# Kernel optimization log

Measured on AMD Instinct MI355X. Metric: run time of the kernel, lower is better.

## Reference

```python
import jax, jax.numpy as jnp
import numpy as np

D_MODEL = 1024
N_HEADS = 16
HEAD_DIM = D_MODEL // N_HEADS
NEG_INF = -1e10


def setup_inputs() -> dict:
    key = jax.random.key(0)
    ks = jax.random.split(key, 6)
    B, S = 2, 2048
    x = jax.random.normal(ks[0], (B, S, D_MODEL), dtype=jnp.float32)
    mask = jnp.ones((B, S), dtype=jnp.int32)
    scale_w = 1.0 / np.sqrt(D_MODEL)
    Wq = jax.random.normal(ks[1], (D_MODEL, D_MODEL), dtype=jnp.float32) * scale_w
    Wk = jax.random.normal(ks[2], (D_MODEL, D_MODEL), dtype=jnp.float32) * scale_w
    Wv = jax.random.normal(ks[3], (D_MODEL, D_MODEL), dtype=jnp.float32) * scale_w
    Wo = jax.random.normal(ks[4], (D_MODEL, D_MODEL), dtype=jnp.float32) * scale_w
    bq = jnp.zeros((D_MODEL,), jnp.float32)
    bk = jnp.zeros((D_MODEL,), jnp.float32)
    bv = jnp.zeros((D_MODEL,), jnp.float32)
    bo = jnp.zeros((D_MODEL,), jnp.float32)
    return {"x": x, "mask": mask, "Wq": Wq, "bq": bq, "Wk": Wk, "bk": bk,
            "Wv": Wv, "bv": bv, "Wo": Wo, "bo": bo}


def reference(x, mask, Wq, bq, Wk, bk, Wv, bv, Wo, bo):
    B, S, _ = x.shape
    # Linear projections (torch Linear: y = x @ W.T + b)
    Q = x @ Wq.T + bq
    K = x @ Wk.T + bk
    V = x @ Wv.T + bv
    # [B, H, S, Dh]
    Q = Q.reshape(B, S, N_HEADS, HEAD_DIM).transpose(0, 2, 1, 3)
    K = K.reshape(B, S, N_HEADS, HEAD_DIM).transpose(0, 2, 1, 3)
    V = V.reshape(B, S, N_HEADS, HEAD_DIM).transpose(0, 2, 1, 3)
    scale = jnp.sqrt(jnp.float32(HEAD_DIM))
    energy = jnp.einsum('bhqd,bhkd->bhqk', Q, K) / scale  # [B,H,S,S]
    # mask: [B,S] -> broadcast over heads and query dim (keys masked)
    m = mask[:, None, None, :]  # [B,1,1,S]
    energy = jnp.where(m == 0, jnp.float32(NEG_INF), energy)
    attention = jax.nn.softmax(energy, axis=-1)
    # dropout in eval mode = identity
    out = jnp.einsum('bhqk,bhkd->bhqd', attention, V)  # [B,H,S,Dh]
    out = out.transpose(0, 2, 1, 3).reshape(B, S, D_MODEL)
    return out @ Wo.T + bo
```

## Files before the change

### kernel.cpp

```cpp
#include <hip/hip_runtime.h>
#include <hip/hip_bf16.h>

typedef __hip_bfloat16 bf16;
typedef __attribute__((ext_vector_type(8))) short s8v;
typedef __attribute__((ext_vector_type(4))) float f4v;

#define D_MODEL 1024
#define S_LEN   2048
#define BATCH   2
#define NH      16
#define HD      64
#define M_TOTAL 4096
#define NT      (S_LEN / 64)

__device__ __forceinline__ void gll16(const bf16* g, bf16* l) {
    __builtin_amdgcn_global_load_lds(
        (const __attribute__((address_space(1))) void*)g,
        (__attribute__((address_space(3))) void*)l, 16, 0, 0);
}

__global__ __launch_bounds__(256) void cvt_bf16x8(const float* __restrict__ s,
                                                  bf16* __restrict__ d, int n) {
    int i = (blockIdx.x * 256 + threadIdx.x) * 8;
    if (i < n) {
        float4 a = *(const float4*)(s + i);
        float4 b = *(const float4*)(s + i + 4);
        union { bf16 h[8]; uint4 u; } p;
        p.h[0] = __float2bfloat16(a.x); p.h[1] = __float2bfloat16(a.y);
        p.h[2] = __float2bfloat16(a.z); p.h[3] = __float2bfloat16(a.w);
        p.h[4] = __float2bfloat16(b.x); p.h[5] = __float2bfloat16(b.y);
        p.h[6] = __float2bfloat16(b.z); p.h[7] = __float2bfloat16(b.w);
        *(uint4*)(d + i) = p.u;
    }
}

struct WPtrs { const float* s0; const float* s1; const float* s2; const float* s3;
               bf16* d0; bf16* d1; bf16* d2; bf16* d3; };

__global__ __launch_bounds__(256) void cvt_w(WPtrs p) {
    const float* s; bf16* d;
    switch (blockIdx.y) {
        case 0:  s = p.s0; d = p.d0; break;
        case 1:  s = p.s1; d = p.d1; break;
        case 2:  s = p.s2; d = p.d2; break;
        default: s = p.s3; d = p.d3; break;
    }
    int i = (blockIdx.x * 256 + threadIdx.x) * 8;
    float4 a = *(const float4*)(s + i);
    float4 b = *(const float4*)(s + i + 4);
    union { bf16 h[8]; uint4 u; } q;
    q.h[0] = __float2bfloat16(a.x); q.h[1] = __float2bfloat16(a.y);
    q.h[2] = __float2bfloat16(a.z); q.h[3] = __float2bfloat16(a.w);
    q.h[4] = __float2bfloat16(b.x); q.h[5] = __float2bfloat16(b.y);
    q.h[6] = __float2bfloat16(b.z); q.h[7] = __float2bfloat16(b.w);
    *(uint4*)(d + i) = q.u;
}

template<int TM, int TN>
__device__ __forceinline__ void gemm_main(const bf16* __restrict__ A,
                                          const bf16* __restrict__ W,
                                          bf16* As, bf16* Bs,
                                          int bm, int bn,
                                          f4v (&acc)[TM/32][TN/32])
{
    constexpr int FM = TM / 32, FN = TN / 32;
    constexpr int CALLS_A = TM / 16, CALLS = (TM + TN) / 16, PW = CALLS / 4;
    const int t = threadIdx.x, wv = t >> 6, lane = t & 63;
    const int quad = lane >> 4, l15 = lane & 15;
    const int wm = (wv >> 1) * (TM / 2), wn = (wv & 1) * (TN / 2);
    const int lr = lane >> 2, lc = (lane & 3) * 8;

    auto STAGE = [&](int buf, int k0) {
        #pragma unroll
        for (int c = 0; c < PW; ++c) {
            const int cc = wv * PW + c;
            if (cc < CALLS_A) {
                gll16(A + (size_t)(bm + cc * 16 + lr) * D_MODEL + k0 + lc,
                      As + buf * (TM * 32) + cc * 16 * 32);
            } else {
                const int r2 = cc - CALLS_A;
                gll16(W + (size_t)(bn + r2 * 16 + lr) * D_MODEL + k0 + lc,
                      Bs + buf * (TN * 32) + r2 * 16 * 32);
            }
        }
    };

    STAGE(0, 0);
    __syncthreads();
    int cur = 0;

    for (int k0 = 0; k0 < D_MODEL; k0 += 32) {
        if (k0 + 32 < D_MODEL) STAGE(cur ^ 1, k0 + 32);

        const bf16* ab = As + cur * (TM * 32);
        const bf16* bb = Bs + cur * (TN * 32);
        s8v af[FM], bfv[FN];
        #pragma unroll
        for (int i = 0; i < FM; ++i)
            af[i] = *(const s8v*)(ab + (wm + i * 16 + l15) * 32 + quad * 8);
        #pragma unroll
        for (int j = 0; j < FN; ++j)
            bfv[j] = *(const s8v*)(bb + (wn + j * 16 + l15) * 32 + quad * 8);
        __builtin_amdgcn_s_setprio(1);
        #pragma unroll
        for (int i = 0; i < FM; ++i)
            #pragma unroll
            for (int j = 0; j < FN; ++j)
                acc[i][j] = __builtin_amdgcn_mfma_f32_16x16x32_bf16(af[i], bfv[j], acc[i][j], 0, 0, 0);
        __builtin_amdgcn_s_setprio(0);

        __syncthreads();
        cur ^= 1;
    }
}

__global__ __launch_bounds__(256) void gemm_qkv(
    const bf16* __restrict__ x,
    const bf16* __restrict__ Wq, const bf16* __restrict__ Wk, const bf16* __restrict__ Wv,
    const float* __restrict__ bq, const float* __restrict__ bk, const float* __restrict__ bv,
    bf16* __restrict__ Qb, bf16* __restrict__ Kb, bf16* __restrict__ Vtb)
{
    __shared__ __align__(16) char smem[4 * 64 * 72 * 2];
    bf16* As = (bf16*)smem;
    bf16* Bs = (bf16*)(smem + 2 * 128 * 32 * 2);
    bf16 (*Tw)[64][72] = (bf16(*)[64][72])smem;

    const int z = blockIdx.z;
    const bf16*  W    = (z == 0) ? Wq : (z == 1) ? Wk : Wv;
    const float* bias = (z == 0) ? bq : (z == 1) ? bk : bv;
    bf16*        out  = (z == 0) ? Qb : (z == 1) ? Kb : Vtb;
    const int bm = blockIdx.y * 128, bn = blockIdx.x * 128;

    f4v acc[4][4] = {};
    gemm_main<128, 128>(x, W, As, Bs, bm, bn, acc);

    const int t = threadIdx.x, wv = t >> 6, lane = t & 63;
    const int quad = lane >> 4, l15 = lane & 15;
    const int wm = (wv >> 1) * 64, wn = (wv & 1) * 64;

    if (z == 2) {
        __syncthreads();
        #pragma unroll
        for (int j = 0; j < 4; ++j) {
            const int col = bn + wn + j * 16 + l15;
            const float bv_ = bias[col];
            #pragma unroll
            for (int i = 0; i < 4; ++i) {
                #pragma unroll
                for (int rp = 0; rp < 4; rp += 2) {
                    union { bf16 h[2]; unsigned u; } p2;
                    p2.h[0] = __float2bfloat16(acc[i][j][rp]     + bv_);
                    p2.h[1] = __float2bfloat16(acc[i][j][rp + 1] + bv_);
                    *(unsigned*)&Tw[wv][j * 16 + l15][i * 16 + quad * 4 + rp] = p2.u;
                }
            }
        }
        const int bb = (bm + wm) >> 11, s0 = (bm + wm) & 2047;
        #pragma unroll
        for (int p = 0; p < 8; ++p) {
            const int dl = p * 8 + (lane >> 3);
            const int sl = (lane & 7) * 8;
            const int col = bn + wn + dl;
            const int h = col >> 6, d = col & 63;
            uint4 v = *(const uint4*)&Tw[wv][dl][sl];
            *(uint4*)&out[(((size_t)(bb * NH + h)) * HD + d) * S_LEN + s0 + sl] = v;
        }
    } else {
        #pragma unroll
        for (int j = 0; j < 4; ++j) {
            const int col = bn + wn + j * 16 + l15;
            const float bv_ = bias[col];
            const int h = col >> 6, d = col & 63;
            #pragma unroll
            for (int i = 0; i < 4; ++i) {
                #pragma unroll
                for (int r = 0; r < 4; ++r) {
                    const int row = bm + wm + i * 16 + quad * 4 + r;
                    const int b = row >> 11, s = row & 2047;
                    const float v = acc[i][j][r] + bv_;
                    out[(((size_t)(b * NH + h)) * S_LEN + s) * HD + d] = __float2bfloat16(v);
                }
            }
        }
    }
}

__global__ __launch_bounds__(256) void gemm_out(
    const bf16* __restrict__ Ob, const bf16* __restrict__ Wo,
    const float* __restrict__ bo, float* __restrict__ out)
{
    __shared__ __align__(16) bf16 As[2][64 * 32];
    __shared__ __align__(16) bf16 Bs[2][128 * 32];
    const int bm = blockIdx.y * 64, bn = blockIdx.x * 128;

    f4v acc[2][4] = {};
    gemm_main<64, 128>(Ob, Wo, &As[0][0], &Bs[0][0], bm, bn, acc);

    const int t = threadIdx.x, wv = t >> 6, lane = t & 63;
    const int quad = lane >> 4, l15 = lane & 15;
    const int wm = (wv >> 1) * 32, wn = (wv & 1) * 64;
    #pragma unroll
    for (int j = 0; j < 4; ++j) {
        const int col = bn + wn + j * 16 + l15;
        const float bv_ = bo[col];
        #pragma unroll
        for (int i = 0; i < 2; ++i)
            #pragma unroll
            for (int r = 0; r < 4; ++r) {
                const int row = bm + wm + i * 16 + quad * 4 + r;
                out[(size_t)row * D_MODEL + col] = acc[i][j][r] + bv_;
            }
    }
}

__global__ __launch_bounds__(256) void attn_mfma(
    const bf16* __restrict__ Q, const bf16* __restrict__ K,
    const bf16* __restrict__ Vt, const int* __restrict__ mask,
    bf16* __restrict__ O)
{
    __shared__ __align__(16) bf16 Ks[2][64][64];
    __shared__ __align__(16) bf16 Vts[2][64][64];
    __shared__ __align__(16) bf16 Ps[4][16][64];

    const int t = threadIdx.x, wv = t >> 6, lane = t & 63;
    const int quad = lane >> 4, l15 = lane & 15;
    const int sw = l15 & 7;
    const int bid = blockIdx.x;
    const int b = bid & 1, h = (bid >> 1) & 15, qt = bid >> 5;
    const int q0 = qt * 64;
    const size_t qkbase = ((size_t)(b * NH + h)) * S_LEN * HD;
    const size_t vtbase = ((size_t)(b * NH + h)) * HD * S_LEN;

    const float KSC  = 0.125f * 1.44269504f;
    const float THR2 = 8.0f * 1.44269504f;

    const bf16* qrow = Q + qkbase + (size_t)(q0 + wv * 16 + l15) * HD;
    const s8v qf0 = *(const s8v*)(qrow + quad * 8);
    const s8v qf1 = *(const s8v*)(qrow + 32 + quad * 8);

    const int grl = lane >> 3, gch = (lane & 7) ^ grl;
    auto STAGEKV = [&](int bf, int kt2) {
        const int k0s = kt2 * 64;
        #pragma unroll
        for (int g = 0; g < 2; ++g) {
            const int r0 = wv * 16 + g * 8;
            gll16(K  + qkbase + (size_t)(k0s + r0 + grl) * HD + gch * 8,
                  &Ks[bf][r0][0]);
            gll16(Vt + vtbase + (size_t)(r0 + grl) * S_LEN + k0s + gch * 8,
                  &Vts[bf][r0][0]);
        }
    };

    STAGEKV(0, 0);
    __syncthreads();

    float mprev = -1e30f, lsum = 0.f;
    f4v oacc[4] = {};
    int cur = 0;

    for (int kt = 0; kt < NT; ++kt) {
        const int k0 = kt * 64;
        const bool more = (kt + 1 < NT);
        if (more) STAGEKV(cur ^ 1, kt + 1);

        int4 mk[4];
        #pragma unroll
        for (int c = 0; c < 4; ++c)
            mk[c] = *(const int4*)&mask[b * S_LEN + k0 + c * 16 + quad * 4];

        const char* kbase = (const char*)&Ks[cur][0][0];
        const char* vbase = (const char*)&Vts[cur][0][0];

        f4v st[4];
        __builtin_amdgcn_s_setprio(1);
        #pragma unroll
        for (int c = 0; c < 4; ++c) {
            const char* kr = kbase + (c * 16 + l15) * 128;
            s8v kf0 = *(const s8v*)(kr + ((quad ^ sw) << 4));
            s8v kf1 = *(const s8v*)(kr + (((4 + quad) ^ sw) << 4));
            f4v z = {0.f, 0.f, 0.f, 0.f};
            z = __builtin_amdgcn_mfma_f32_16x16x32_bf16(kf0, qf0, z, 0, 0, 0);
            z = __builtin_amdgcn_mfma_f32_16x16x32_bf16(kf1, qf1, z, 0, 0, 0);
            st[c] = z;
        }
        __builtin_amdgcn_s_setprio(0);

        float mt = -1e30f;
        #pragma unroll
        for (int c = 0; c < 4; ++c) {
            f4v m4;
            m4[0] = mk[c].x ? 0.f : -1e30f;
            m4[1] = mk[c].y ? 0.f : -1e30f;
            m4[2] = mk[c].z ? 0.f : -1e30f;
            m4[3] = mk[c].w ? 0.f : -1e30f;
            st[c] = st[c] * KSC + m4;
            mt = fmaxf(mt, fmaxf(fmaxf(st[c][0], st[c][1]), fmaxf(st[c][2], st[c][3])));
        }
        mt = fmaxf(mt, __shfl_xor(mt, 16, 64));
        mt = fmaxf(mt, __shfl_xor(mt, 32, 64));

        float mn = mprev;
        if (!__all(mt <= mprev + THR2)) {
            mn = fmaxf(mprev, mt);
            const float alpha = __builtin_amdgcn_exp2f(mprev - mn);
            mprev = mn;
            float av[4];
            #pragma unroll
            for (int r = 0; r < 4; ++r) av[r] = __shfl(alpha, quad * 4 + r, 64);
            #pragma unroll
            for (int dt = 0; dt < 4; ++dt)
                #pragma unroll
                for (int r = 0; r < 4; ++r) oacc[dt][r] *= av[r];
            lsum *= alpha;
        }

        f4v psv = {0.f, 0.f, 0.f, 0.f};
        #pragma unroll
        for (int c = 0; c < 4; ++c) {
            f4v e = st[c] - mn;
            e[0] = __builtin_amdgcn_exp2f(e[0]);
            e[1] = __builtin_amdgcn_exp2f(e[1]);
            e[2] = __builtin_amdgcn_exp2f(e[2]);
            e[3] = __builtin_amdgcn_exp2f(e[3]);
            st[c] = e;
            psv += e;
        }
        lsum += psv[0] + psv[1] + psv[2] + psv[3];

        char* pr = (char*)&Ps[wv][l15][0];
        #pragma unroll
        for (int c = 0; c < 4; ++c) {
            union { bf16 hh[4]; short4 s4; } pk;
            pk.hh[0] = __float2bfloat16(st[c][0]);
            pk.hh[1] = __float2bfloat16(st[c][1]);
            pk.hh[2] = __float2bfloat16(st[c][2]);
            pk.hh[3] = __float2bfloat16(st[c][3]);
            const int wch = (2 * c + (quad >> 1)) ^ sw;
            *(short4*)(pr + (wch << 4) + ((quad & 1) << 3)) = pk.s4;
        }
        s8v pf0 = *(const s8v*)(pr + ((quad ^ sw) << 4));
        s8v pf1 = *(const s8v*)(pr + (((4 + quad) ^ sw) << 4));

        __builtin_amdgcn_s_setprio(1);
        #pragma unroll
        for (int dt = 0; dt < 4; ++dt) {
            const char* vr = vbase + (dt * 16 + l15) * 128;
            s8v vf0 = *(const s8v*)(vr + ((quad ^ sw) << 4));
            s8v vf1 = *(const s8v*)(vr + (((4 + quad) ^ sw) << 4));
            oacc[dt] = __builtin_amdgcn_mfma_f32_16x16x32_bf16(pf0, vf0, oacc[dt], 0, 0, 0);
            oacc[dt] = __builtin_amdgcn_mfma_f32_16x16x32_bf16(pf1, vf1, oacc[dt], 0, 0, 0);
        }
        __builtin_amdgcn_s_setprio(0);

        if (more) __syncthreads();
        cur ^= 1;
    }

    lsum += __shfl_xor(lsum, 16, 64);
    lsum += __shfl_xor(lsum, 32, 64);
    float linv[4];
    #pragma unroll
    for (int r = 0; r < 4; ++r) linv[r] = 1.f / __shfl(lsum, quad * 4 + r, 64);
    #pragma unroll
    for (int dt = 0; dt < 4; ++dt) {
        #pragma unroll
        for (int r = 0; r < 4; ++r) {
            const int s = q0 + wv * 16 + quad * 4 + r;
            const int col = h * 64 + dt * 16 + l15;
            O[((size_t)b * S_LEN + s) * D_MODEL + col] = __float2bfloat16(oacc[dt][r] * linv[r]);
        }
    }
}

extern "C" void kernel_launch(void* const* d_in, const int* in_sizes, int n_in,
                              void* d_out, int out_size, void* d_ws, size_t ws_size,
                              hipStream_t stream) {
    const float* x    = (const float*)d_in[0];
    const int*   mask = (const int*)  d_in[1];
    const float* Wq   = (const float*)d_in[2];
    const float* bq   = (const float*)d_in[3];
    const float* Wk   = (const float*)d_in[4];
    const float* bk   = (const float*)d_in[5];
    const float* Wv   = (const float*)d_in[6];
    const float* bv   = (const float*)d_in[7];
    const float* Wo   = (const float*)d_in[8];
    const float* bo   = (const float*)d_in[9];
    float* out = (float*)d_out;

    char* w = (char*)d_ws;
    bf16* xb  = (bf16*)w; w += (size_t)M_TOTAL * D_MODEL * 2;
    bf16* Wqb = (bf16*)w; w += (size_t)D_MODEL * D_MODEL * 2;
    bf16* Wkb = (bf16*)w; w += (size_t)D_MODEL * D_MODEL * 2;
    bf16* Wvb = (bf16*)w; w += (size_t)D_MODEL * D_MODEL * 2;
    bf16* Wob = (bf16*)w; w += (size_t)D_MODEL * D_MODEL * 2;
    bf16* Qb  = (bf16*)w; w += (size_t)M_TOTAL * D_MODEL * 2;
    bf16* Kb  = (bf16*)w; w += (size_t)M_TOTAL * D_MODEL * 2;
    bf16* Vtb = (bf16*)w; w += (size_t)M_TOTAL * D_MODEL * 2;
    bf16* Ob  = (bf16*)w; w += (size_t)M_TOTAL * D_MODEL * 2;

    const int nx = M_TOTAL * D_MODEL;
    cvt_bf16x8<<<nx / 2048, 256, 0, stream>>>(x, xb, nx);
    WPtrs wp = { Wq, Wk, Wv, Wo, Wqb, Wkb, Wvb, Wob };
    cvt_w<<<dim3(D_MODEL * D_MODEL / 2048, 4), 256, 0, stream>>>(wp);

    gemm_qkv<<<dim3(8, 32, 3), 256, 0, stream>>>(xb, Wqb, Wkb, Wvb, bq, bk, bv, Qb, Kb, Vtb);

    attn_mfma<<<BATCH * NH * (S_LEN / 64), 256, 0, stream>>>(Qb, Kb, Vtb, mask, Ob);

    gemm_out<<<dim3(8, 64), 256, 0, stream>>>(Ob, Wob, bo, out);
}
```

Before: 241.6 us.

## Prefetch K/V tiles into registers with single LDS buffer in attention

Replaces the double-buffered global_load_lds staging of K and V tiles with a register prefetch. The next tile is loaded into VGPRs during compute and written to a single LDS buffer at the top of each iteration, between two barriers. The mask is also staged once per tile into shared memory as additive floats, replacing the per-lane int4 global loads. This halves K/V LDS use, which may raise occupancy, but adds registers, an extra barrier per iteration and explicit LDS stores.

Result: faster. 222.4 us (-7.9%).

```diff
diff --git a/kernel.cpp b/kernel.cpp
--- a/kernel.cpp
+++ b/kernel.cpp
@@ -218,9 +218,10 @@
     const bf16* __restrict__ Vt, const int* __restrict__ mask,
     bf16* __restrict__ O)
 {
-    __shared__ __align__(16) bf16 Ks[2][64][64];
-    __shared__ __align__(16) bf16 Vts[2][64][64];
+    __shared__ __align__(16) bf16 Ks[64][64];
+    __shared__ __align__(16) bf16 Vts[64][64];
     __shared__ __align__(16) bf16 Ps[4][16][64];
+    __shared__ float mb[64];
 
     const int t = threadIdx.x, wv = t >> 6, lane = t & 63;
     const int quad = lane >> 4, l15 = lane & 15;
@@ -238,44 +239,44 @@
     const s8v qf0 = *(const s8v*)(qrow + quad * 8);
     const s8v qf1 = *(const s8v*)(qrow + 32 + quad * 8);
 
-    const int grl = lane >> 3, gch = (lane & 7) ^ grl;
-    auto STAGEKV = [&](int bf, int kt2) {
-        const int k0s = kt2 * 64;
-        #pragma unroll
-        for (int g = 0; g < 2; ++g) {
-            const int r0 = wv * 16 + g * 8;
-            gll16(K  + qkbase + (size_t)(k0s + r0 + grl) * HD + gch * 8,
-                  &Ks[bf][r0][0]);
-            gll16(Vt + vtbase + (size_t)(r0 + grl) * S_LEN + k0s + gch * 8,
-                  &Vts[bf][r0][0]);
-        }
+    const int srow = t >> 2;
+    const int swr  = srow & 7;
+    const int c2   = (t & 3) * 2;
+    const int ch0  = c2 ^ swr, ch1 = (c2 + 1) ^ swr;
+
+    uint4 kr0, kr1, vr0, vr1; int mr = 1;
+    auto LOADT = [&](int kt2) {
+        const int kk = kt2 * 64;
+        const uint4* kp = (const uint4*)(K  + qkbase + (size_t)(kk + srow) * HD + c2 * 8);
+        const uint4* vp = (const uint4*)(Vt + vtbase + (size_t)srow * S_LEN + kk + c2 * 8);
+        kr0 = kp[0]; kr1 = kp[1];
+        vr0 = vp[0]; vr1 = vp[1];
+        if (t < 64) mr = mask[b * S_LEN + kk + t];
     };
-
-    STAGEKV(0, 0);
-    __syncthreads();
+    auto STAGE = [&]() {
+        *(uint4*)&Ks[srow][ch0 * 8]  = kr0;
+        *(uint4*)&Ks[srow][ch1 * 8]  = kr1;
+        *(uint4*)&Vts[srow][ch0 * 8] = vr0;
+        *(uint4*)&Vts[srow][ch1 * 8] = vr1;
+        if (t < 64) mb[t] = mr ? 0.f : -1e30f;
+    };
+
+    LOADT(0);
 
     float mprev = -1e30f, lsum = 0.f;
     f4v oacc[4] = {};
-    int cur = 0;
 
     for (int kt = 0; kt < NT; ++kt) {
-        const int k0 = kt * 64;
-        const bool more = (kt + 1 < NT);
-        if (more) STAGEKV(cur ^ 1, kt + 1);
-
-        int4 mk[4];
-        #pragma unroll
-        for (int c = 0; c < 4; ++c)
-            mk[c] = *(const int4*)&mask[b * S_LEN + k0 + c * 16 + quad * 4];
-
-        const char* kbase = (const char*)&Ks[cur][0][0];
-        const char* vbase = (const char*)&Vts[cur][0][0];
+        __syncthreads();
+        STAGE();
+        __syncthreads();
+        if (kt + 1 < NT) LOADT(kt + 1);
 
         f4v st[4];
         __builtin_amdgcn_s_setprio(1);
         #pragma unroll
         for (int c = 0; c < 4; ++c) {
-            const char* kr = kbase + (c * 16 + l15) * 128;
+            const char* kr = (const char*)&Ks[c * 16 + l15][0];
             s8v kf0 = *(const s8v*)(kr + ((quad ^ sw) << 4));
             s8v kf1 = *(const s8v*)(kr + (((4 + quad) ^ sw) << 4));
             f4v z = {0.f, 0.f, 0.f, 0.f};
@@ -288,11 +289,7 @@
         float mt = -1e30f;
         #pragma unroll
         for (int c = 0; c < 4; ++c) {
-            f4v m4;
-            m4[0] = mk[c].x ? 0.f : -1e30f;
-            m4[1] = mk[c].y ? 0.f : -1e30f;
-            m4[2] = mk[c].z ? 0.f : -1e30f;
-            m4[3] = mk[c].w ? 0.f : -1e30f;
+            const f4v m4 = *(const f4v*)&mb[c * 16 + quad * 4];
             st[c] = st[c] * KSC + m4;
             mt = fmaxf(mt, fmaxf(fmaxf(st[c][0], st[c][1]), fmaxf(st[c][2], st[c][3])));
         }
@@ -344,16 +341,13 @@
         __builtin_amdgcn_s_setprio(1);
         #pragma unroll
         for (int dt = 0; dt < 4; ++dt) {
-            const char* vr = vbase + (dt * 16 + l15) * 128;
+            const char* vr = (const char*)&Vts[dt * 16 + l15][0];
             s8v vf0 = *(const s8v*)(vr + ((quad ^ sw) << 4));
             s8v vf1 = *(const s8v*)(vr + (((4 + quad) ^ sw) << 4));
             oacc[dt] = __builtin_amdgcn_mfma_f32_16x16x32_bf16(pf0, vf0, oacc[dt], 0, 0, 0);
             oacc[dt] = __builtin_amdgcn_mfma_f32_16x16x32_bf16(pf1, vf1, oacc[dt], 0, 0, 0);
         }
         __builtin_amdgcn_s_setprio(0);
-
-        if (more) __syncthreads();
-        cur ^= 1;
     }
 
     lsum += __shfl_xor(lsum, 16, 64);
```
